# Kernel tuning notes

Hardware: AMD Instinct MI355X
Metric: run time of the kernel (lower is better)

## Reference

```python
import jax, jax.numpy as jnp
import numpy as np

EMBED = 256
HEADS = 8
HEAD_DIM = 32
MLP_DIM = 1024
NEG = -1e9  # large negative in place of -inf so fully-deselected rows don't NaN
LN_EPS = 1e-5


def _layernorm(x, g, b):
    m = jnp.mean(x, axis=-1, keepdims=True)
    v = jnp.mean(jnp.square(x - m), axis=-1, keepdims=True)
    return (x - m) / jnp.sqrt(v + LN_EPS) * g + b


def setup_inputs() -> dict:
    key = jax.random.key(0)
    ks = jax.random.split(key, 16)
    b, s, d = 64, 360, EMBED
    sc = 0.02
    return {
        "x": jax.random.normal(ks[0], (b, s, d), dtype=jnp.float32),
        "attention_mask": jnp.zeros((b, 1, 1, s), dtype=jnp.float32),
        # TokenRouter.weight_predictor: Linear(256, 1)
        "wp_w": jax.random.normal(ks[1], (1, d), dtype=jnp.float32) * sc,
        "wp_b": jnp.zeros((1,), dtype=jnp.float32),
        # TokenRouter.aux_predictor: Linear(256,128) -> SiLU -> Linear(128,2)
        "a1_w": jax.random.normal(ks[2], (d // 2, d), dtype=jnp.float32) * sc,
        "a1_b": jnp.zeros((d // 2,), dtype=jnp.float32),
        "a2_w": jax.random.normal(ks[3], (2, d // 2), dtype=jnp.float32) * sc,
        "a2_b": jnp.zeros((2,), dtype=jnp.float32),
        # transformer block (pre-LN GPT2-style)
        "ln1_g": jnp.ones((d,), dtype=jnp.float32),
        "ln1_b": jnp.zeros((d,), dtype=jnp.float32),
        "wqkv": jax.random.normal(ks[4], (d, 3 * d), dtype=jnp.float32) * sc,
        "bqkv": jnp.zeros((3 * d,), dtype=jnp.float32),
        "wo": jax.random.normal(ks[5], (d, d), dtype=jnp.float32) * sc,
        "bo": jnp.zeros((d,), dtype=jnp.float32),
        "ln2_g": jnp.ones((d,), dtype=jnp.float32),
        "ln2_b": jnp.zeros((d,), dtype=jnp.float32),
        "w1": jax.random.normal(ks[6], (d, MLP_DIM), dtype=jnp.float32) * sc,
        "b1": jnp.zeros((MLP_DIM,), dtype=jnp.float32),
        "w2": jax.random.normal(ks[7], (MLP_DIM, d), dtype=jnp.float32) * sc,
        "b2": jnp.zeros((d,), dtype=jnp.float32),
    }


def reference(x, attention_mask, wp_w, wp_b, a1_w, a1_b, a2_w, a2_b,
              ln1_g, ln1_b, wqkv, bqkv, wo, bo, ln2_g, ln2_b, w1, b1, w2, b2):
    b, s, d = x.shape
    # --- router: per-token scalar weight ---
    weights = (x @ wp_w.T + wp_b).squeeze(-1)  # [b, s]
    # --- aux predictor selects tokens (eval path: argmax over 2 logits) ---
    h = jax.nn.silu(x @ a1_w.T + a1_b)
    aux_logits = h @ a2_w.T + a2_b            # [b, s, 2]
    sel = jnp.argmax(aux_logits, axis=-1).astype(bool)  # [b, s]
    # --- masked transformer block over the selected token subset.
    # Compacting tokens then attending == full-seq attention with deselected
    # keys masked out (LN/MLP/residual are position-wise), so vectorize:
    bias = attention_mask + jnp.where(sel, 0.0, NEG)[:, None, None, :]  # [b,1,1,s]
    hn = _layernorm(x, ln1_g, ln1_b)
    qkv = hn @ wqkv + bqkv
    q, k, v = jnp.split(qkv, 3, axis=-1)
    q = q.reshape(b, s, HEADS, HEAD_DIM)
    k = k.reshape(b, s, HEADS, HEAD_DIM)
    v = v.reshape(b, s, HEADS, HEAD_DIM)
    scores = jnp.einsum("bqhd,bkhd->bhqk", q, k) / np.sqrt(HEAD_DIM).astype(np.float32)
    scores = scores + bias                   # [b, h, s, s]
    attn = jax.nn.softmax(scores, axis=-1)
    ctx = jnp.einsum("bhqk,bkhd->bqhd", attn, v).reshape(b, s, d)
    h1 = x + (ctx @ wo + bo)
    h2n = _layernorm(h1, ln2_g, ln2_b)
    block_out = h1 + (jax.nn.gelu(h2n @ w1 + b1) @ w2 + b2)  # [b, s, d]
    # --- scatter-recombine: selected -> weighted block output, else passthrough
    out = jnp.where(sel[..., None], block_out * weights[..., None], x)
    avg_selected = jnp.sum(sel.astype(x.dtype)) / b
    return out, avg_selected
```

## Files before the change

### kernel.cpp

```cpp
#include <hip/hip_runtime.h>
#include <math.h>
#include <stdint.h>

#define TOKN 23040
#define BSZ 64
#define SEQ 360
#define DIM 256
#define NHD 8
#define HDD 32
#define MLPD 1024
#define NEGV -1e9f

typedef __attribute__((ext_vector_type(8))) short bf16x8;
typedef __attribute__((ext_vector_type(4))) float f32x4;

static __device__ __forceinline__ short f2bs(float f) {
  unsigned u = __builtin_bit_cast(unsigned, f);
  u += 0x7fffu + ((u >> 16) & 1u);
  return (short)(u >> 16);
}
static __device__ __forceinline__ unsigned packbf(float a, float b) {
  return (unsigned)(unsigned short)f2bs(a) | ((unsigned)(unsigned short)f2bs(b) << 16);
}

__global__ __launch_bounds__(256) void convw_k(
    const float* __restrict__ wqkv, const float* __restrict__ wo,
    const float* __restrict__ w1, const float* __restrict__ w2,
    short* __restrict__ wqkvt, short* __restrict__ wot,
    short* __restrict__ w1t, short* __restrict__ w2t) {
  int id = blockIdx.x * 256 + threadIdx.x;
  if (id < 256 * 768) {
    int k = id / 768, n = id % 768;
    wqkvt[n * 256 + k] = f2bs(wqkv[id]);
  }
  if (id < 256 * 256) {
    int k = id >> 8, n = id & 255;
    wot[n * 256 + k] = f2bs(wo[id]);
  }
  if (id < 256 * 1024) {
    int k = id >> 10, n = id & 1023;
    w1t[n * 256 + k] = f2bs(w1[id]);
  }
  if (id < 1024 * 256) {
    int k = id >> 8, n = id & 255;
    w2t[n * 1024 + k] = f2bs(w2[id]);
  }
}

__global__ __launch_bounds__(64) void ln_router_k(
    const float* __restrict__ in, const float* __restrict__ g,
    const float* __restrict__ b, const float* __restrict__ wpw,
    const float* __restrict__ wpb, short* __restrict__ outn,
    float* __restrict__ wout, float* __restrict__ outx) {
  int tok = blockIdx.x, lane = threadIdx.x;
  const float4 xv = *(const float4*)(in + (size_t)tok * DIM + lane * 4);
  *(float4*)(outx + (size_t)tok * DIM + lane * 4) = xv;
  float s = xv.x + xv.y + xv.z + xv.w;
  float s2 = xv.x * xv.x + xv.y * xv.y + xv.z * xv.z + xv.w * xv.w;
#pragma unroll
  for (int o = 1; o < 64; o <<= 1) { s += __shfl_xor(s, o); s2 += __shfl_xor(s2, o); }
  float m = s * (1.f / DIM);
  float var = fmaxf(s2 * (1.f / DIM) - m * m, 0.f);
  float rstd = rsqrtf(var + 1e-5f);
  float4 gv = *(const float4*)(g + lane * 4);
  float4 bv = *(const float4*)(b + lane * 4);
  uint2 pk;
  pk.x = packbf((xv.x - m) * rstd * gv.x + bv.x, (xv.y - m) * rstd * gv.y + bv.y);
  pk.y = packbf((xv.z - m) * rstd * gv.z + bv.z, (xv.w - m) * rstd * gv.w + bv.w);
  *(uint2*)(outn + (size_t)tok * DIM + lane * 4) = pk;
  float4 wv = *(const float4*)(wpw + lane * 4);
  float wd = xv.x * wv.x + xv.y * wv.y + xv.z * wv.z + xv.w * wv.w;
#pragma unroll
  for (int o = 1; o < 64; o <<= 1) wd += __shfl_xor(wd, o);
  if (lane == 0) wout[tok] = wd + wpb[0];
}

__global__ __launch_bounds__(64) void ln_k(
    const float* __restrict__ in, const float* __restrict__ g,
    const float* __restrict__ b, const int* __restrict__ mtotp,
    short* __restrict__ outn) {
  int tok = blockIdx.x, lane = threadIdx.x;
  if (tok >= *mtotp) return;
  const float4 xv = *(const float4*)(in + (size_t)tok * DIM + lane * 4);
  float s = xv.x + xv.y + xv.z + xv.w;
  float s2 = xv.x * xv.x + xv.y * xv.y + xv.z * xv.z + xv.w * xv.w;
#pragma unroll
  for (int o = 1; o < 64; o <<= 1) { s += __shfl_xor(s, o); s2 += __shfl_xor(s2, o); }
  float m = s * (1.f / DIM);
  float var = fmaxf(s2 * (1.f / DIM) - m * m, 0.f);
  float rstd = rsqrtf(var + 1e-5f);
  float4 gv = *(const float4*)(g + lane * 4);
  float4 bv = *(const float4*)(b + lane * 4);
  uint2 pk;
  pk.x = packbf((xv.x - m) * rstd * gv.x + bv.x, (xv.y - m) * rstd * gv.y + bv.y);
  pk.y = packbf((xv.z - m) * rstd * gv.z + bv.z, (xv.w - m) * rstd * gv.w + bv.w);
  *(uint2*)(outn + (size_t)tok * DIM + lane * 4) = pk;
}

__global__ __launch_bounds__(256) void router_gemm_k(
    const float* __restrict__ x, const float* __restrict__ a1w,
    const float* __restrict__ a1b, float* __restrict__ H) {
  __shared__ __align__(16) float Xs[64][36];
  __shared__ __align__(16) float Ws[128][36];
  int m0 = blockIdx.x * 64;
  int t = threadIdx.x;
  int tx = t & 31, ty = t >> 5;
  float acc[8][4] = {};
  int r = t >> 2, c = (t & 3) * 8;
  int r2 = t >> 1, c2 = (t & 1) * 16;
  for (int k0 = 0; k0 < 256; k0 += 32) {
    *(float4*)&Xs[r][c] = *(const float4*)(x + (size_t)(m0 + r) * 256 + k0 + c);
    *(float4*)&Xs[r][c + 4] = *(const float4*)(x + (size_t)(m0 + r) * 256 + k0 + c + 4);
#pragma unroll
    for (int j = 0; j < 4; j++)
      *(float4*)&Ws[r2][c2 + j * 4] =
          *(const float4*)(a1w + (size_t)r2 * 256 + k0 + c2 + j * 4);
    __syncthreads();
    for (int kk = 0; kk < 32; kk++) {
      float wv[4], xv8[8];
#pragma unroll
      for (int j = 0; j < 4; j++) wv[j] = Ws[tx * 4 + j][kk];
#pragma unroll
      for (int i = 0; i < 8; i++) xv8[i] = Xs[ty * 8 + i][kk];
#pragma unroll
      for (int i = 0; i < 8; i++)
#pragma unroll
        for (int j = 0; j < 4; j++) acc[i][j] += xv8[i] * wv[j];
    }
    __syncthreads();
  }
#pragma unroll
  for (int i = 0; i < 8; i++)
#pragma unroll
    for (int j = 0; j < 4; j++) {
      int row = m0 + ty * 8 + i, dim = tx * 4 + j;
      float v = acc[i][j] + a1b[dim];
      float sg = 1.f / (1.f + expf(-v));
      H[(size_t)row * 128 + dim] = v * sg;
    }
}

__global__ __launch_bounds__(64) void router2_k(
    const float* __restrict__ H, const float* __restrict__ a2w,
    const float* __restrict__ a2b, int* __restrict__ sel) {
  int tok = blockIdx.x, lane = threadIdx.x;
  float h0 = H[(size_t)tok * 128 + lane];
  float h1 = H[(size_t)tok * 128 + 64 + lane];
  float l0 = h0 * a2w[lane] + h1 * a2w[64 + lane];
  float l1 = h0 * a2w[128 + lane] + h1 * a2w[192 + lane];
#pragma unroll
  for (int o = 1; o < 64; o <<= 1) { l0 += __shfl_xor(l0, o); l1 += __shfl_xor(l1, o); }
  if (lane == 0) {
    l0 += a2b[0]; l1 += a2b[1];
    sel[tok] = (l1 > l0) ? 1 : 0;
  }
}

__global__ __launch_bounds__(512) void scanA_k(const int* __restrict__ sel,
                                               int* __restrict__ idxl,
                                               int* __restrict__ cnt) {
  __shared__ int sc[512];
  int b = blockIdx.x, t = threadIdx.x;
  int flag = (t < SEQ) ? sel[b * SEQ + t] : 0;
  sc[t] = flag;
  __syncthreads();
  int val = flag;
  for (int off = 1; off < 512; off <<= 1) {
    int add = (t >= off) ? sc[t - off] : 0;
    __syncthreads();
    val += add;
    sc[t] = val;
    __syncthreads();
  }
  if (flag) idxl[b * SEQ + (val - 1)] = t;
  if (t == 511) cnt[b] = val;
}

__global__ __launch_bounds__(512) void scanB_k(const int* __restrict__ cnt,
                                               int* __restrict__ startp,
                                               int* __restrict__ mtotp,
                                               int* __restrict__ g_idx) {
  __shared__ int sc[64];
  int t = threadIdx.x;
  if (t < 64) sc[t] = cnt[t];
  __syncthreads();
  if (t == 0) {
    int run = 0;
    for (int b = 0; b < 64; b++) { startp[b] = run; run += sc[b]; }
    *mtotp = run;
  }
  for (int i = t; i < TOKN; i += 512) g_idx[i] = 0;
}

__global__ __launch_bounds__(512) void scanC_k(const int* __restrict__ idxl,
                                               const int* __restrict__ startp,
                                               const int* __restrict__ cnt,
                                               int* __restrict__ g_idx) {
  int b = blockIdx.x, t = threadIdx.x;
  int c = cnt[b], s0 = startp[b];
  for (int j = t; j < c; j += 512) g_idx[s0 + j] = b * SEQ + idxl[b * SEQ + j];
}

__global__ __launch_bounds__(256) void finalize_k(const int* __restrict__ sel,
                                                  float* __restrict__ outavg) {
  __shared__ int wsum[4];
  int t = threadIdx.x;
  int s = 0;
  for (int i = t; i < TOKN; i += 256) s += sel[i];
#pragma unroll
  for (int o = 1; o < 64; o <<= 1) s += __shfl_xor(s, o);
  if ((t & 63) == 0) wsum[t >> 6] = s;
  __syncthreads();
  if (t == 0) outavg[0] = (float)(wsum[0] + wsum[1] + wsum[2] + wsum[3]) / 64.0f;
}

template <int MODE>
__global__ __launch_bounds__(256) void gemm_bt_k(
    const short* __restrict__ A, const short* __restrict__ Bt,
    const float* __restrict__ bias, const float* __restrict__ res,
    const float* __restrict__ wgt, const int* __restrict__ g_idx,
    const int* __restrict__ mtotp, short* __restrict__ outb,
    float* __restrict__ outf, int Ndim, int Kdim) {
  int Mt = *mtotp;
  int m0 = blockIdx.y * 64;
  if (m0 >= Mt) return;
  __shared__ __align__(16) short As[64][40];
  __shared__ __align__(16) short Bs[64][40];
  int n0 = blockIdx.x * 64;
  int t = threadIdx.x;
  int wave = t >> 6, lane = t & 63;
  int l15 = lane & 15, quad = lane >> 4;
  int wr = (wave >> 1) * 32, wc = (wave & 1) * 32;
  int srow = t >> 2, scg = (t & 3) * 8;
  int arow = (MODE == 0) ? g_idx[m0 + srow] : (m0 + srow);

  f32x4 acc[2][2];
#pragma unroll
  for (int i = 0; i < 2; i++)
#pragma unroll
    for (int j = 0; j < 2; j++)
#pragma unroll
      for (int r = 0; r < 4; r++) acc[i][j][r] = 0.f;

  for (int k0 = 0; k0 < Kdim; k0 += 32) {
    int4 av = *(const int4*)(A + (size_t)arow * Kdim + k0 + scg);
    int4 bv = *(const int4*)(Bt + (size_t)(n0 + srow) * Kdim + k0 + scg);
    *(int4*)&As[srow][scg] = av;
    *(int4*)&Bs[srow][scg] = bv;
    __syncthreads();
    bf16x8 af[2], bfr[2];
    af[0] = *(const bf16x8*)&As[wr + l15][quad * 8];
    af[1] = *(const bf16x8*)&As[wr + 16 + l15][quad * 8];
    bfr[0] = *(const bf16x8*)&Bs[wc + l15][quad * 8];
    bfr[1] = *(const bf16x8*)&Bs[wc + 16 + l15][quad * 8];
#pragma unroll
    for (int i = 0; i < 2; i++)
#pragma unroll
      for (int j = 0; j < 2; j++)
        acc[i][j] = __builtin_amdgcn_mfma_f32_16x16x32_bf16(af[i], bfr[j],
                                                            acc[i][j], 0, 0, 0);
    __syncthreads();
  }

#pragma unroll
  for (int i = 0; i < 2; i++)
#pragma unroll
    for (int j = 0; j < 2; j++) {
      int col = n0 + wc + j * 16 + l15;
      float bcol = bias[col];
#pragma unroll
      for (int r = 0; r < 4; r++) {
        int row = m0 + wr + i * 16 + quad * 4 + r;
        float v = acc[i][j][r] + bcol;
        size_t idx = (size_t)row * Ndim + col;
        if (MODE == 0) {
          outb[idx] = f2bs(v);
        } else if (MODE == 1) {
          int orig = g_idx[row];
          outf[idx] = v + res[(size_t)orig * 256 + col];
        } else if (MODE == 2) {
          float u = 0.7978845608028654f * (v + 0.044715f * v * v * v);
          float e = __expf(2.f * u);
          float th = 1.f - 2.f / (e + 1.f);
          outb[idx] = f2bs(0.5f * v * (1.f + th));
        } else {
          if (row < Mt) {
            int orig = g_idx[row];
            float o = (v + res[idx]) * wgt[orig];
            outf[(size_t)orig * 256 + col] = o;
          }
        }
      }
    }
}

__global__ __launch_bounds__(256) void attn_k(
    const short* __restrict__ qkv, const float* __restrict__ amask,
    const int* __restrict__ g_idx, const int* __restrict__ startp,
    const int* __restrict__ cntp, short* __restrict__ ctx) {
  __shared__ __align__(16) short VF[2 * 12 * 64 * 8];
  __shared__ __align__(16) float ls[384];
  int bh = blockIdx.x >> 1, qhalf = blockIdx.x & 1;
  int bb = bh >> 3, h = bh & 7;
  int t = threadIdx.x;
  int start = startp[bb], cnt = cntp[bb];
  size_t base = (size_t)start * 768;
  for (int i = t; i < 1536; i += 256) {
    int k = i >> 2, cg = (i & 3) * 8;
    union { int4 v; short s[8]; } u;
    if (k < cnt) {
      u.v = *(const int4*)(qkv + base + (size_t)k * 768 + 512 + h * 32 + cg);
    } else {
      u.v = make_int4(0, 0, 0, 0);
    }
    int c = k >> 5, qd = (k >> 3) & 3, j = k & 7;
#pragma unroll
    for (int jj = 0; jj < 8; jj++) {
      int d = cg + jj;
      VF[((((d >> 4) * 12 + c) * 64) + qd * 16 + (d & 15)) * 8 + j] = u.s[jj];
    }
  }
  for (int i = t; i < 384; i += 256)
    ls[i] = (i < cnt) ? amask[g_idx[start + i]] : 0.f;
  __syncthreads();

  int wave = t >> 6, lane = t & 63;
  int ql = lane & 15, quad = lane >> 4;
  int addr0 = (((quad & 1) * 2) * 16 + ql) * 4;
  int addr1 = addr0 + 64;
  bool hiq = quad >= 2;
  int nt = (cnt + 15) >> 4;
  int nc = (cnt + 31) >> 5;

  for (int qt = qhalf + 2 * wave; qt < nt; qt += 8) {
    int q0 = qt * 16, qrow = q0 + ql;
    bf16x8 qf;
#pragma unroll
    for (int j = 0; j < 8; j++) qf[j] = 0;
    if (qrow < cnt)
      qf = *(const bf16x8*)(qkv + base + (size_t)qrow * 768 + h * 32 + quad * 8);

    f32x4 o0, o1;
#pragma unroll
    for (int r = 0; r < 4; r++) { o0[r] = 0.f; o1[r] = 0.f; }
    float lsum = 0.f;

    for (int c = 0; c < nc; c++) {
      int keyA = c * 32 + ql;
      int keyB = keyA + 16;
      bf16x8 kfA, kfB;
#pragma unroll
      for (int j = 0; j < 8; j++) { kfA[j] = 0; kfB[j] = 0; }
      if (keyA < cnt)
        kfA = *(const bf16x8*)(qkv + base + (size_t)keyA * 768 + 256 + h * 32 + quad * 8);
      if (keyB < cnt)
        kfB = *(const bf16x8*)(qkv + base + (size_t)keyB * 768 + 256 + h * 32 + quad * 8);
      f32x4 sa, sb;
#pragma unroll
      for (int r = 0; r < 4; r++) { sa[r] = 0.f; sb[r] = 0.f; }
      sa = __builtin_amdgcn_mfma_f32_16x16x32_bf16(kfA, qf, sa, 0, 0, 0);
      sb = __builtin_amdgcn_mfma_f32_16x16x32_bf16(kfB, qf, sb, 0, 0, 0);
      int kbase = c * 32 + quad * 4;
      float4 la = *(const float4*)&ls[kbase];
      float4 lb = *(const float4*)&ls[kbase + 16];
      float ea0 = (kbase + 0 < cnt) ? __expf(sa[0] * 0.17677669529663687f + la.x) : 0.f;
      float ea1 = (kbase + 1 < cnt) ? __expf(sa[1] * 0.17677669529663687f + la.y) : 0.f;
      float ea2 = (kbase + 2 < cnt) ? __expf(sa[2] * 0.17677669529663687f + la.z) : 0.f;
      float ea3 = (kbase + 3 < cnt) ? __expf(sa[3] * 0.17677669529663687f + la.w) : 0.f;
      float eb0 = (kbase + 16 < cnt) ? __expf(sb[0] * 0.17677669529663687f + lb.x) : 0.f;
      float eb1 = (kbase + 17 < cnt) ? __expf(sb[1] * 0.17677669529663687f + lb.y) : 0.f;
      float eb2 = (kbase + 18 < cnt) ? __expf(sb[2] * 0.17677669529663687f + lb.z) : 0.f;
      float eb3 = (kbase + 19 < cnt) ? __expf(sb[3] * 0.17677669529663687f + lb.w) : 0.f;
      lsum += (ea0 + ea1) + (ea2 + ea3) + (eb0 + eb1) + (eb2 + eb3);
      unsigned pA0 = packbf(ea0, ea1), pA1 = packbf(ea2, ea3);
      unsigned pB0 = packbf(eb0, eb1), pB1 = packbf(eb2, eb3);
      int s00 = __builtin_amdgcn_ds_bpermute(addr0, (int)pA0);
      int s10 = __builtin_amdgcn_ds_bpermute(addr0, (int)pB0);
      int s01 = __builtin_amdgcn_ds_bpermute(addr0, (int)pA1);
      int s11 = __builtin_amdgcn_ds_bpermute(addr0, (int)pB1);
      int s02 = __builtin_amdgcn_ds_bpermute(addr1, (int)pA0);
      int s12 = __builtin_amdgcn_ds_bpermute(addr1, (int)pB0);
      int s03 = __builtin_amdgcn_ds_bpermute(addr1, (int)pA1);
      int s13 = __builtin_amdgcn_ds_bpermute(addr1, (int)pB1);
      union { int i[4]; bf16x8 v; } pf;
      pf.i[0] = hiq ? s10 : s00;
      pf.i[1] = hiq ? s11 : s01;
      pf.i[2] = hiq ? s12 : s02;
      pf.i[3] = hiq ? s13 : s03;
      bf16x8 v0 = *(const bf16x8*)&VF[(c * 64 + lane) * 8];
      bf16x8 v1 = *(const bf16x8*)&VF[((12 + c) * 64 + lane) * 8];
      o0 = __builtin_amdgcn_mfma_f32_16x16x32_bf16(v0, pf.v, o0, 0, 0, 0);
      o1 = __builtin_amdgcn_mfma_f32_16x16x32_bf16(v1, pf.v, o1, 0, 0, 0);
    }
    lsum += __shfl_xor(lsum, 16);
    lsum += __shfl_xor(lsum, 32);
    float inv = 1.f / lsum;

    if (qrow < cnt) {
      size_t cb = ((size_t)(start + qrow)) * 256 + h * 32;
      uint2 w0, w1;
      w0.x = packbf(o0[0] * inv, o0[1] * inv);
      w0.y = packbf(o0[2] * inv, o0[3] * inv);
      w1.x = packbf(o1[0] * inv, o1[1] * inv);
      w1.y = packbf(o1[2] * inv, o1[3] * inv);
      *(uint2*)(ctx + cb + quad * 4) = w0;
      *(uint2*)(ctx + cb + 16 + quad * 4) = w1;
    }
  }
}

extern "C" void kernel_launch(void* const* d_in, const int* in_sizes, int n_in,
                              void* d_out, int out_size, void* d_ws,
                              size_t ws_size, hipStream_t stream) {
  const float* x = (const float*)d_in[0];
  const float* amask = (const float*)d_in[1];
  const float* wp_w = (const float*)d_in[2];
  const float* wp_b = (const float*)d_in[3];
  const float* a1_w = (const float*)d_in[4];
  const float* a1_b = (const float*)d_in[5];
  const float* a2_w = (const float*)d_in[6];
  const float* a2_b = (const float*)d_in[7];
  const float* ln1_g = (const float*)d_in[8];
  const float* ln1_b = (const float*)d_in[9];
  const float* wqkv = (const float*)d_in[10];
  const float* bqkv = (const float*)d_in[11];
  const float* wo = (const float*)d_in[12];
  const float* bo = (const float*)d_in[13];
  const float* ln2_g = (const float*)d_in[14];
  const float* ln2_b = (const float*)d_in[15];
  const float* w1 = (const float*)d_in[16];
  const float* b1 = (const float*)d_in[17];
  const float* w2 = (const float*)d_in[18];
  const float* b2 = (const float*)d_in[19];
  float* out = (float*)d_out;

  uint8_t* p = (uint8_t*)d_ws;
  float* weightsv = (float*)p; p += (size_t)TOKN * 4;
  int* selv = (int*)p;         p += (size_t)TOKN * 4;
  int* idxlv = (int*)p;        p += (size_t)TOKN * 4;
  int* gidxv = (int*)p;        p += (size_t)TOKN * 4;
  int* cntv = (int*)p;         p += 64 * 4;
  int* startv = (int*)p;       p += 64 * 4;
  int* mtotv = (int*)p;        p += 64 * 4;
  short* wqkvt = (short*)p;    p += (size_t)768 * 256 * 2;
  short* wot = (short*)p;      p += (size_t)256 * 256 * 2;
  short* w1t = (short*)p;      p += (size_t)1024 * 256 * 2;
  short* w2t = (short*)p;      p += (size_t)256 * 1024 * 2;
  float* h1v = (float*)p;      p += (size_t)TOKN * 256 * 4;
  short* h2nv = (short*)p;     p += (size_t)TOKN * 256 * 2;
  uint8_t* ctxH = p;           p += (size_t)TOKN * 256 * 2;
  short* ctxv = (short*)ctxH;
  float* Hv = (float*)ctxH;
  uint8_t* R = p;
  short* xnv = (short*)R;
  short* qkvv = (short*)(R + (size_t)TOKN * 256 * 2);
  short* actv = (short*)R;

  convw_k<<<dim3(1024), dim3(256), 0, stream>>>(wqkv, wo, w1, w2, wqkvt, wot, w1t, w2t);
  ln_router_k<<<dim3(TOKN), dim3(64), 0, stream>>>(x, ln1_g, ln1_b, wp_w, wp_b, xnv,
                                                   weightsv, out);
  router_gemm_k<<<dim3(360), dim3(256), 0, stream>>>(x, a1_w, a1_b, Hv);
  router2_k<<<dim3(TOKN), dim3(64), 0, stream>>>(Hv, a2_w, a2_b, selv);
  scanA_k<<<dim3(64), dim3(512), 0, stream>>>(selv, idxlv, cntv);
  scanB_k<<<dim3(1), dim3(512), 0, stream>>>(cntv, startv, mtotv, gidxv);
  scanC_k<<<dim3(64), dim3(512), 0, stream>>>(idxlv, startv, cntv, gidxv);
  finalize_k<<<dim3(1), dim3(256), 0, stream>>>(selv, out + (size_t)TOKN * 256);
  gemm_bt_k<0><<<dim3(12, 360), dim3(256), 0, stream>>>(
      xnv, wqkvt, bqkv, nullptr, nullptr, gidxv, mtotv, qkvv, nullptr, 768, 256);
  attn_k<<<dim3(1024), dim3(256), 0, stream>>>(qkvv, amask, gidxv, startv, cntv, ctxv);
  gemm_bt_k<1><<<dim3(4, 360), dim3(256), 0, stream>>>(
      ctxv, wot, bo, x, nullptr, gidxv, mtotv, nullptr, h1v, 256, 256);
  ln_k<<<dim3(TOKN), dim3(64), 0, stream>>>(h1v, ln2_g, ln2_b, mtotv, h2nv);
  gemm_bt_k<2><<<dim3(16, 360), dim3(256), 0, stream>>>(
      h2nv, w1t, b1, nullptr, nullptr, gidxv, mtotv, actv, nullptr, 1024, 256);
  gemm_bt_k<3><<<dim3(4, 360), dim3(256), 0, stream>>>(
      actv, w2t, b2, h1v, weightsv, gidxv, mtotv, nullptr, out, 256, 1024);
}
```

Measured before the change: 289.0 us.

## Fuse router second layer into router GEMM and pack LN kernels four tokens per block

Folds the SiLU and the 128->2 logit projection into the router GEMM epilogue, reducing across lanes with shuffles. This removes the intermediate H buffer round trip and one launch. The avg-selected count moves into scanB from the total count, which drops the finalize kernel. The LN kernels now run four tokens per 256-thread block instead of one per 64-thread block, and router GEMM shared tiles are transposed so the inner loop uses vector LDS reads. The transposed stores may add LDS bank conflicts.

```diff
diff --git a/kernel.cpp b/kernel.cpp
--- a/kernel.cpp
+++ b/kernel.cpp
@@ -47,12 +47,13 @@
   }
 }
 
-__global__ __launch_bounds__(64) void ln_router_k(
+__global__ __launch_bounds__(256) void ln_router_k(
     const float* __restrict__ in, const float* __restrict__ g,
     const float* __restrict__ b, const float* __restrict__ wpw,
     const float* __restrict__ wpb, short* __restrict__ outn,
     float* __restrict__ wout, float* __restrict__ outx) {
-  int tok = blockIdx.x, lane = threadIdx.x;
+  int tok = blockIdx.x * 4 + (threadIdx.x >> 6);
+  int lane = threadIdx.x & 63;
   const float4 xv = *(const float4*)(in + (size_t)tok * DIM + lane * 4);
   *(float4*)(outx + (size_t)tok * DIM + lane * 4) = xv;
   float s = xv.x + xv.y + xv.z + xv.w;
@@ -75,11 +76,12 @@
   if (lane == 0) wout[tok] = wd + wpb[0];
 }
 
-__global__ __launch_bounds__(64) void ln_k(
+__global__ __launch_bounds__(256) void ln_k(
     const float* __restrict__ in, const float* __restrict__ g,
     const float* __restrict__ b, const int* __restrict__ mtotp,
     short* __restrict__ outn) {
-  int tok = blockIdx.x, lane = threadIdx.x;
+  int tok = blockIdx.x * 4 + (threadIdx.x >> 6);
+  int lane = threadIdx.x & 63;
   if (tok >= *mtotp) return;
   const float4 xv = *(const float4*)(in + (size_t)tok * DIM + lane * 4);
   float s = xv.x + xv.y + xv.z + xv.w;
@@ -99,60 +101,66 @@
 
 __global__ __launch_bounds__(256) void router_gemm_k(
     const float* __restrict__ x, const float* __restrict__ a1w,
-    const float* __restrict__ a1b, float* __restrict__ H) {
-  __shared__ __align__(16) float Xs[64][36];
-  __shared__ __align__(16) float Ws[128][36];
+    const float* __restrict__ a1b, const float* __restrict__ a2w,
+    const float* __restrict__ a2b, int* __restrict__ sel) {
+  __shared__ __align__(16) float XT[32][65];
+  __shared__ __align__(16) float WT[32][128];
   int m0 = blockIdx.x * 64;
   int t = threadIdx.x;
   int tx = t & 31, ty = t >> 5;
   float acc[8][4] = {};
   int r = t >> 2, c = (t & 3) * 8;
-  int r2 = t >> 1, c2 = (t & 1) * 16;
+  int n2 = t >> 1, c2 = (t & 1) * 16;
   for (int k0 = 0; k0 < 256; k0 += 32) {
-    *(float4*)&Xs[r][c] = *(const float4*)(x + (size_t)(m0 + r) * 256 + k0 + c);
-    *(float4*)&Xs[r][c + 4] = *(const float4*)(x + (size_t)(m0 + r) * 256 + k0 + c + 4);
-#pragma unroll
-    for (int j = 0; j < 4; j++)
-      *(float4*)&Ws[r2][c2 + j * 4] =
-          *(const float4*)(a1w + (size_t)r2 * 256 + k0 + c2 + j * 4);
-    __syncthreads();
+    float4 xa = *(const float4*)(x + (size_t)(m0 + r) * 256 + k0 + c);
+    float4 xb = *(const float4*)(x + (size_t)(m0 + r) * 256 + k0 + c + 4);
+    XT[c + 0][r] = xa.x; XT[c + 1][r] = xa.y; XT[c + 2][r] = xa.z; XT[c + 3][r] = xa.w;
+    XT[c + 4][r] = xb.x; XT[c + 5][r] = xb.y; XT[c + 6][r] = xb.z; XT[c + 7][r] = xb.w;
+#pragma unroll
+    for (int j = 0; j < 4; j++) {
+      float4 wv = *(const float4*)(a1w + (size_t)n2 * 256 + k0 + c2 + j * 4);
+      WT[c2 + j * 4 + 0][n2] = wv.x;
+      WT[c2 + j * 4 + 1][n2] = wv.y;
+      WT[c2 + j * 4 + 2][n2] = wv.z;
+      WT[c2 + j * 4 + 3][n2] = wv.w;
+    }
+    __syncthreads();
+#pragma unroll 8
     for (int kk = 0; kk < 32; kk++) {
-      float wv[4], xv8[8];
-#pragma unroll
-      for (int j = 0; j < 4; j++) wv[j] = Ws[tx * 4 + j][kk];
-#pragma unroll
-      for (int i = 0; i < 8; i++) xv8[i] = Xs[ty * 8 + i][kk];
+      float4 wv4 = *(const float4*)&WT[kk][tx * 4];
+      float4 x0 = *(const float4*)&XT[kk][ty * 8];
+      float4 x1 = *(const float4*)&XT[kk][ty * 8 + 4];
+      float xr[8] = {x0.x, x0.y, x0.z, x0.w, x1.x, x1.y, x1.z, x1.w};
+      float wr[4] = {wv4.x, wv4.y, wv4.z, wv4.w};
 #pragma unroll
       for (int i = 0; i < 8; i++)
 #pragma unroll
-        for (int j = 0; j < 4; j++) acc[i][j] += xv8[i] * wv[j];
-    }
-    __syncthreads();
-  }
-#pragma unroll
-  for (int i = 0; i < 8; i++)
+        for (int j = 0; j < 4; j++) acc[i][j] += xr[i] * wr[j];
+    }
+    __syncthreads();
+  }
+  float b1v[4], a20[4], a21[4];
+#pragma unroll
+  for (int j = 0; j < 4; j++) {
+    int dim = tx * 4 + j;
+    b1v[j] = a1b[dim];
+    a20[j] = a2w[dim];
+    a21[j] = a2w[128 + dim];
+  }
+  float bias0 = a2b[0], bias1 = a2b[1];
+#pragma unroll
+  for (int i = 0; i < 8; i++) {
+    float l0 = 0.f, l1 = 0.f;
 #pragma unroll
     for (int j = 0; j < 4; j++) {
-      int row = m0 + ty * 8 + i, dim = tx * 4 + j;
-      float v = acc[i][j] + a1b[dim];
-      float sg = 1.f / (1.f + expf(-v));
-      H[(size_t)row * 128 + dim] = v * sg;
-    }
-}
-
-__global__ __launch_bounds__(64) void router2_k(
-    const float* __restrict__ H, const float* __restrict__ a2w,
-    const float* __restrict__ a2b, int* __restrict__ sel) {
-  int tok = blockIdx.x, lane = threadIdx.x;
-  float h0 = H[(size_t)tok * 128 + lane];
-  float h1 = H[(size_t)tok * 128 + 64 + lane];
-  float l0 = h0 * a2w[lane] + h1 * a2w[64 + lane];
-  float l1 = h0 * a2w[128 + lane] + h1 * a2w[192 + lane];
-#pragma unroll
-  for (int o = 1; o < 64; o <<= 1) { l0 += __shfl_xor(l0, o); l1 += __shfl_xor(l1, o); }
-  if (lane == 0) {
-    l0 += a2b[0]; l1 += a2b[1];
-    sel[tok] = (l1 > l0) ? 1 : 0;
+      float v = acc[i][j] + b1v[j];
+      float h = v / (1.f + expf(-v));
+      l0 += h * a20[j];
+      l1 += h * a21[j];
+    }
+#pragma unroll
+    for (int o = 1; o < 32; o <<= 1) { l0 += __shfl_xor(l0, o); l1 += __shfl_xor(l1, o); }
+    if (tx == 0) sel[m0 + ty * 8 + i] = (l1 + bias1 > l0 + bias0) ? 1 : 0;
   }
 }
 
@@ -179,7 +187,8 @@
 __global__ __launch_bounds__(512) void scanB_k(const int* __restrict__ cnt,
                                                int* __restrict__ startp,
                                                int* __restrict__ mtotp,
-                                               int* __restrict__ g_idx) {
+                                               int* __restrict__ g_idx,
+                                               float* __restrict__ outavg) {
   __shared__ int sc[64];
   int t = threadIdx.x;
   if (t < 64) sc[t] = cnt[t];
@@ -188,6 +197,7 @@
     int run = 0;
     for (int b = 0; b < 64; b++) { startp[b] = run; run += sc[b]; }
     *mtotp = run;
+    outavg[0] = (float)run / 64.0f;
   }
   for (int i = t; i < TOKN; i += 512) g_idx[i] = 0;
 }
@@ -199,19 +209,6 @@
   int b = blockIdx.x, t = threadIdx.x;
   int c = cnt[b], s0 = startp[b];
   for (int j = t; j < c; j += 512) g_idx[s0 + j] = b * SEQ + idxl[b * SEQ + j];
-}
-
-__global__ __launch_bounds__(256) void finalize_k(const int* __restrict__ sel,
-                                                  float* __restrict__ outavg) {
-  __shared__ int wsum[4];
-  int t = threadIdx.x;
-  int s = 0;
-  for (int i = t; i < TOKN; i += 256) s += sel[i];
-#pragma unroll
-  for (int o = 1; o < 64; o <<= 1) s += __shfl_xor(s, o);
-  if ((t & 63) == 0) wsum[t >> 6] = s;
-  __syncthreads();
-  if (t == 0) outavg[0] = (float)(wsum[0] + wsum[1] + wsum[2] + wsum[3]) / 64.0f;
 }
 
 template <int MODE>
@@ -448,29 +445,26 @@
   short* w2t = (short*)p;      p += (size_t)256 * 1024 * 2;
   float* h1v = (float*)p;      p += (size_t)TOKN * 256 * 4;
   short* h2nv = (short*)p;     p += (size_t)TOKN * 256 * 2;
-  uint8_t* ctxH = p;           p += (size_t)TOKN * 256 * 2;
-  short* ctxv = (short*)ctxH;
-  float* Hv = (float*)ctxH;
+  short* ctxv = (short*)p;     p += (size_t)TOKN * 256 * 2;
   uint8_t* R = p;
   short* xnv = (short*)R;
   short* qkvv = (short*)(R + (size_t)TOKN * 256 * 2);
   short* actv = (short*)R;
 
   convw_k<<<dim3(1024), dim3(256), 0, stream>>>(wqkv, wo, w1, w2, wqkvt, wot, w1t, w2t);
-  ln_router_k<<<dim3(TOKN), dim3(64), 0, stream>>>(x, ln1_g, ln1_b, wp_w, wp_b, xnv,
-                                                   weightsv, out);
-  router_gemm_k<<<dim3(360), dim3(256), 0, stream>>>(x, a1_w, a1_b, Hv);
-  router2_k<<<dim3(TOKN), dim3(64), 0, stream>>>(Hv, a2_w, a2_b, selv);
+  ln_router_k<<<dim3(TOKN / 4), dim3(256), 0, stream>>>(x, ln1_g, ln1_b, wp_w, wp_b,
+                                                        xnv, weightsv, out);
+  router_gemm_k<<<dim3(360), dim3(256), 0, stream>>>(x, a1_w, a1_b, a2_w, a2_b, selv);
   scanA_k<<<dim3(64), dim3(512), 0, stream>>>(selv, idxlv, cntv);
-  scanB_k<<<dim3(1), dim3(512), 0, stream>>>(cntv, startv, mtotv, gidxv);
+  scanB_k<<<dim3(1), dim3(512), 0, stream>>>(cntv, startv, mtotv, gidxv,
+                                             out + (size_t)TOKN * 256);
   scanC_k<<<dim3(64), dim3(512), 0, stream>>>(idxlv, startv, cntv, gidxv);
-  finalize_k<<<dim3(1), dim3(256), 0, stream>>>(selv, out + (size_t)TOKN * 256);
   gemm_bt_k<0><<<dim3(12, 360), dim3(256), 0, stream>>>(
       xnv, wqkvt, bqkv, nullptr, nullptr, gidxv, mtotv, qkvv, nullptr, 768, 256);
   attn_k<<<dim3(1024), dim3(256), 0, stream>>>(qkvv, amask, gidxv, startv, cntv, ctxv);
   gemm_bt_k<1><<<dim3(4, 360), dim3(256), 0, stream>>>(
       ctxv, wot, bo, x, nullptr, gidxv, mtotv, nullptr, h1v, 256, 256);
-  ln_k<<<dim3(TOKN), dim3(64), 0, stream>>>(h1v, ln2_g, ln2_b, mtotv, h2nv);
+  ln_k<<<dim3(TOKN / 4), dim3(256), 0, stream>>>(h1v, ln2_g, ln2_b, mtotv, h2nv);
   gemm_bt_k<2><<<dim3(16, 360), dim3(256), 0, stream>>>(
       h2nv, w1t, b1, nullptr, nullptr, gidxv, mtotv, actv, nullptr, 1024, 256);
   gemm_bt_k<3><<<dim3(4, 360), dim3(256), 0, stream>>>(
```

After: 261.3 us. 1.11x faster.
